# Optimization experiments

Hardware: AMD Instinct MI355X
Metric: run time of the kernel (lower is better)

## Reference

```python
import jax, jax.numpy as jnp
import numpy as np

B, C, W, H, Z = 2, 32, 96, 96, 64
IC = C  # inter_channels defaults to in_channels (required by depthwise g conv)
THRESH = 1.5
EPS = 1e-5


def setup_inputs() -> dict:
    key = jax.random.key(0)
    ks = jax.random.split(key, 12)
    s1 = 1.0 / np.sqrt(C)   # 1x1x1 conv fan-in
    s3 = 1.0 / np.sqrt(3.0) # depthwise (1,1,3) conv fan-in per channel
    return {
        "x": jax.random.normal(ks[0], (B, C, W, H, Z), jnp.float32),
        # per-sample spacings in [0,3): mixes both branches around thresh 1.5
        "spacings": jax.random.uniform(ks[1], (B, 3), jnp.float32) * 3.0,
        "theta_w": jax.random.normal(ks[2], (IC, C), jnp.float32) * s1,
        "theta_b": jax.random.normal(ks[3], (IC,), jnp.float32) * s1,
        "phi_w": jax.random.normal(ks[4], (IC, C), jnp.float32) * s1,
        "phi_b": jax.random.normal(ks[5], (IC,), jnp.float32) * s1,
        "g_w": jax.random.normal(ks[6], (C, 3), jnp.float32) * s3,   # depthwise kernel along z
        "g_b": jax.random.normal(ks[7], (C,), jnp.float32) * s3,
        "W_w": jax.random.normal(ks[8], (C, IC), jnp.float32) * s1,
        "W_b": jax.random.normal(ks[9], (C,), jnp.float32) * s1,
        # torch inits BN gamma=0, beta=0 (zero-init residual trick); use small random
        "bn_gamma": jax.random.normal(ks[10], (C,), jnp.float32) * 0.1,
        "bn_beta": jax.random.normal(ks[11], (C,), jnp.float32) * 0.1,
    }


def _cvec(v):
    return v.reshape(1, -1, 1, 1, 1)


def _conv1x1(h, w, b):
    # 1x1x1 Conv3d == channel-mixing matmul
    return jnp.einsum('bcwhz,oc->bowhz', h, w) + _cvec(b)


def reference(x, spacings, theta_w, theta_b, phi_w, phi_b, g_w, g_b, W_w, W_b, bn_gamma, bn_beta):
    # theta/phi: 1x1x1 convs -> (B, IC, W, H, Z)
    t = _conv1x1(x, theta_w, theta_b)
    p = _conv1x1(x, phi_w, phi_b)

    # g: depthwise conv along z, kernel 3, pad 1 (groups=C)
    xp = jnp.pad(x, ((0, 0), (0, 0), (0, 0), (0, 0), (1, 1)))
    gx = (xp[..., :-2] * _cvec(g_w[:, 0])
          + xp[..., 1:-1] * _cvec(g_w[:, 1])
          + xp[..., 2:] * _cvec(g_w[:, 2])
          + _cvec(g_b))

    # non-local attention along z per (b, w, h) row: scores (B, W, H, Z, Z)
    f = jnp.einsum('bcwhz,bcwhy->bwhzy', t, p)
    a = jax.nn.softmax(f, axis=-1)
    y = jnp.einsum('bwhzy,bcwhy->bcwhz', a, gx)
    nl = y + x  # residual inside compute_x

    # per-sample branch on z-spacing, vectorized with where
    mask = (spacings[:, -1] <= THRESH).reshape(-1, 1, 1, 1, 1)
    res = jnp.where(mask, nl, x)

    # W: 1x1x1 conv + BatchNorm3d (training-mode batch stats)
    out = _conv1x1(res, W_w, W_b)
    mean = jnp.mean(out, axis=(0, 2, 3, 4), keepdims=True)
    var = jnp.var(out, axis=(0, 2, 3, 4), keepdims=True)
    out = (out - mean) * jax.lax.rsqrt(var + EPS)
    return out * _cvec(bn_gamma) + _cvec(bn_beta)
```

## Files before the change

### kernel.cpp

```cpp
#include <hip/hip_runtime.h>
#include <stdint.h>

#define CHS 589824
#define ROWS 18432
#define WHn 9216
#define NRED 1179648.0f
#define LOG2E 1.4426950408889634f

typedef short s16x8 __attribute__((ext_vector_type(8)));
typedef float f32x4v __attribute__((ext_vector_type(4)));

#define MFMA16 __builtin_amdgcn_mfma_f32_16x16x32_bf16

#define WSFRAG 10240

#define OXH 0
#define OP  8704
#define OG  13312
#define LDSZ 17664
#define OO  OP
#define OSC OXH

static __device__ __forceinline__ uint16_t bfh(float v) {
    union { __bf16 h; uint16_t u; } c; c.h = (__bf16)v; return c.u;
}
static __device__ __forceinline__ float bf2f(uint16_t u) {
    union { uint32_t x; float f; } c; c.x = (uint32_t)u << 16; return c.f;
}
static __device__ __forceinline__ uint32_t pk2u(uint16_t a, uint16_t b) {
    return (uint32_t)a | ((uint32_t)b << 16);
}
static __device__ __forceinline__ uint32_t pkbf(float a, float b) {
    return pk2u(bfh(a), bfh(b));
}
static __device__ __forceinline__ float ex2(float x) {
    float r;
    asm("v_exp_f32 %0, %1" : "=v"(r) : "v"(x));
    return r;
}
static __device__ __forceinline__ s16x8 rd8(const char* p) {
    union { uint64_t q[2]; s16x8 s; } v;
    v.q[0] = *(const uint64_t*)p;
    v.q[1] = *(const uint64_t*)(p + 8);
    return v.s;
}

static __device__ __forceinline__ void wfrag2(const float* __restrict__ Wp, int mt, int l15, int kb,
                                              float sc, s16x8& hi, s16x8& lo) {
    const float* p = Wp + (l15 + 16*mt)*32 + 8*kb;
    const float4 f0 = *(const float4*)p;
    const float4 f1 = *(const float4*)(p + 4);
    float f[8] = {f0.x*sc, f0.y*sc, f0.z*sc, f0.w*sc, f1.x*sc, f1.y*sc, f1.z*sc, f1.w*sc};
    union { uint32_t u[4]; s16x8 v; } rh, rl;
    #pragma unroll
    for (int i = 0; i < 4; ++i) {
        const uint16_t h0 = bfh(f[2*i]), h1 = bfh(f[2*i+1]);
        rh.u[i] = pk2u(h0, h1);
        rl.u[i] = pk2u(bfh(f[2*i] - bf2f(h0)), bfh(f[2*i+1] - bf2f(h1)));
    }
    hi = rh.v; lo = rl.v;
}
static __device__ __forceinline__ s16x8 wfragW(const float* __restrict__ Wp, int mt, int l15, int kb) {
    const float* p = Wp + (l15 + 16*mt)*32;
    const float4 f0 = *(const float4*)(p + 4*kb);
    const float4 f1 = *(const float4*)(p + 16 + 4*kb);
    union { uint32_t u[4]; s16x8 v; } r;
    r.u[0] = pkbf(f0.x, f0.y); r.u[1] = pkbf(f0.z, f0.w);
    r.u[2] = pkbf(f1.x, f1.y); r.u[3] = pkbf(f1.z, f1.w);
    return r.v;
}

__global__ __launch_bounds__(256) void k0_frag(
    const float* __restrict__ theta_w, const float* __restrict__ phi_w,
    const float* __restrict__ Ww, char* __restrict__ ws)
{
    const int tid = threadIdx.x;
    const int m = tid >> 7;
    const int r = tid & 127;
    const int mt = r >> 6, l = r & 63;
    s16x8 hi, lo;
    wfrag2(m ? phi_w : theta_w, mt, l & 15, l >> 4, m ? 1.0f : LOG2E, hi, lo);
    *(s16x8*)(ws + m*4096 + (mt*64 + l)*16)        = hi;
    *(s16x8*)(ws + m*4096 + 2048 + (mt*64 + l)*16) = lo;
    if (tid < 128) {
        const int mtw = tid >> 6, lw = tid & 63;
        *(s16x8*)(ws + 8192 + (mtw*64 + lw)*16) = wfragW(Ww, mtw, lw & 15, lw >> 4);
    }
}

__global__ __launch_bounds__(256, 8) void k1_row(
    const float* __restrict__ x, const float* __restrict__ spacings,
    const float* __restrict__ theta_b, const float* __restrict__ phi_b,
    const float* __restrict__ g_w, const float* __restrict__ g_b,
    const float* __restrict__ Wb, const char* __restrict__ frags,
    float* __restrict__ out, float* __restrict__ part)
{
    __shared__ __align__(16) char lds[LDSZ];
    const int t = threadIdx.x;
    const int wv = t >> 6, l = t & 63;
    const int l15 = l & 15, kb = l >> 4;
    const int row = blockIdx.x;
    const int b = row / WHn, wh = row - b*WHn;
    const long base = (long)b*32*CHS + (long)wh*64;
    const int zr = 16*wv + l15;

    float xv[8];
    #pragma unroll
    for (int j = 0; j < 8; ++j) xv[j] = x[base + (long)(8*wv + j)*CHS + l];
    #pragma unroll
    for (int j = 0; j < 4; ++j) {
        const uint16_t h0 = bfh(xv[2*j]), h1 = bfh(xv[2*j+1]);
        *(uint32_t*)(lds + OXH + l*136 + (8*wv + 2*j)*2)      = pk2u(h0, h1);
        *(uint32_t*)(lds + OXH + l*136 + 64 + (8*wv + 2*j)*2) =
            pk2u(bfh(xv[2*j] - bf2f(h0)), bfh(xv[2*j+1] - bf2f(h1)));
    }
    const int pG = 32*(l >> 5) + 8*((l >> 2) & 3) + 4*((l >> 4) & 1) + (l & 3);
    #pragma unroll
    for (int j = 0; j < 8; ++j) {
        const int c = 8*wv + j;
        float xm = __shfl_up(xv[j], 1);   if (l == 0)  xm = 0.f;
        float xp = __shfl_down(xv[j], 1); if (l == 63) xp = 0.f;
        const float g = g_w[3*c]*xm + g_w[3*c+1]*xv[j] + g_w[3*c+2]*xp + g_b[c];
        *(uint16_t*)(lds + OG + c*136 + 2*pG) = bfh(g);
    }
    __syncthreads();

    s16x8 bth, btl;
    {
        const s16x8 bxh = rd8(lds + OXH + zr*136 + 16*kb);
        const s16x8 bxl = rd8(lds + OXH + zr*136 + 64 + 16*kb);
        const s16x8 t0h = *(const s16x8*)(frags + l*16);
        const s16x8 t1h = *(const s16x8*)(frags + 1024 + l*16);
        const s16x8 t0l = *(const s16x8*)(frags + 2048 + l*16);
        const s16x8 t1l = *(const s16x8*)(frags + 3072 + l*16);
        const float4 b0 = *(const float4*)(theta_b + 4*kb);
        const float4 b1 = *(const float4*)(theta_b + 16 + 4*kb);
        f32x4v T0; T0[0]=b0.x*LOG2E; T0[1]=b0.y*LOG2E; T0[2]=b0.z*LOG2E; T0[3]=b0.w*LOG2E;
        f32x4v T1; T1[0]=b1.x*LOG2E; T1[1]=b1.y*LOG2E; T1[2]=b1.z*LOG2E; T1[3]=b1.w*LOG2E;
        T0 = MFMA16(t0h, bxh, T0, 0, 0, 0);
        T0 = MFMA16(t0h, bxl, T0, 0, 0, 0);
        T0 = MFMA16(t0l, bxh, T0, 0, 0, 0);
        T1 = MFMA16(t1h, bxh, T1, 0, 0, 0);
        T1 = MFMA16(t1h, bxl, T1, 0, 0, 0);
        T1 = MFMA16(t1l, bxh, T1, 0, 0, 0);
        const s16x8 p0h = *(const s16x8*)(frags + 4096 + l*16);
        const s16x8 p1h = *(const s16x8*)(frags + 4096 + 1024 + l*16);
        const s16x8 p0l = *(const s16x8*)(frags + 4096 + 2048 + l*16);
        const s16x8 p1l = *(const s16x8*)(frags + 4096 + 3072 + l*16);
        const float4 c0 = *(const float4*)(phi_b + 4*kb);
        const float4 c1 = *(const float4*)(phi_b + 16 + 4*kb);
        f32x4v P0; P0[0]=c0.x; P0[1]=c0.y; P0[2]=c0.z; P0[3]=c0.w;
        f32x4v P1; P1[0]=c1.x; P1[1]=c1.y; P1[2]=c1.z; P1[3]=c1.w;
        P0 = MFMA16(p0h, bxh, P0, 0, 0, 0);
        P0 = MFMA16(p0h, bxl, P0, 0, 0, 0);
        P0 = MFMA16(p0l, bxh, P0, 0, 0, 0);
        P1 = MFMA16(p1h, bxh, P1, 0, 0, 0);
        P1 = MFMA16(p1h, bxl, P1, 0, 0, 0);
        P1 = MFMA16(p1l, bxh, P1, 0, 0, 0);
        union { uint32_t u[2]; uint64_t q; } w;
        w.u[0] = pkbf(P0[0], P0[1]); w.u[1] = pkbf(P0[2], P0[3]);
        *(uint64_t*)(lds + OP + zr*72 + 16*kb) = w.q;
        w.u[0] = pkbf(P1[0], P1[1]); w.u[1] = pkbf(P1[2], P1[3]);
        *(uint64_t*)(lds + OP + zr*72 + 16*kb + 8) = w.q;
        uint16_t h[8];
        #pragma unroll
        for (int r = 0; r < 4; ++r) { h[r] = bfh(T0[r]); h[4+r] = bfh(T1[r]); }
        union { uint32_t u[4]; s16x8 s; } H, L;
        H.u[0] = pk2u(h[0], h[1]); H.u[1] = pk2u(h[2], h[3]);
        H.u[2] = pk2u(h[4], h[5]); H.u[3] = pk2u(h[6], h[7]);
        L.u[0] = pkbf(T0[0]-bf2f(h[0]), T0[1]-bf2f(h[1]));
        L.u[1] = pkbf(T0[2]-bf2f(h[2]), T0[3]-bf2f(h[3]));
        L.u[2] = pkbf(T1[0]-bf2f(h[4]), T1[1]-bf2f(h[5]));
        L.u[3] = pkbf(T1[2]-bf2f(h[6]), T1[3]-bf2f(h[7]));
        bth = H.s; btl = L.s;
    }
    __syncthreads();

    f32x4v Fq[4];
    #pragma unroll
    for (int yt = 0; yt < 4; ++yt) {
        const s16x8 pah = rd8(lds + OP + (16*yt + l15)*72 + 16*kb);
        f32x4v zz; zz[0]=0.f; zz[1]=0.f; zz[2]=0.f; zz[3]=0.f;
        zz = MFMA16(pah, bth, zz, 0, 0, 0);
        zz = MFMA16(pah, btl, zz, 0, 0, 0);
        Fq[yt] = zz;
    }

    s16x8 apk[2];
    float inv;
    {
        float mx = -3.4e38f;
        #pragma unroll
        for (int yt = 0; yt < 4; ++yt)
            #pragma unroll
            for (int r = 0; r < 4; ++r) mx = fmaxf(mx, Fq[yt][r]);
        mx = fmaxf(mx, __shfl_xor(mx, 16));
        mx = fmaxf(mx, __shfl_xor(mx, 32));
        float p[4][4]; float sum = 0.f;
        #pragma unroll
        for (int yt = 0; yt < 4; ++yt)
            #pragma unroll
            for (int r = 0; r < 4; ++r) { p[yt][r] = ex2(Fq[yt][r] - mx); sum += p[yt][r]; }
        sum += __shfl_xor(sum, 16);
        sum += __shfl_xor(sum, 32);
        inv = 1.0f / sum;
        #pragma unroll
        for (int ks = 0; ks < 2; ++ks) {
            union { uint32_t u[4]; s16x8 s; } A;
            A.u[0] = pkbf(p[2*ks][0],   p[2*ks][1]);
            A.u[1] = pkbf(p[2*ks][2],   p[2*ks][3]);
            A.u[2] = pkbf(p[2*ks+1][0], p[2*ks+1][1]);
            A.u[3] = pkbf(p[2*ks+1][2], p[2*ks+1][3]);
            apk[ks] = A.s;
        }
    }

    s16x8 brf;
    {
        f32x4v Yq[2];
        #pragma unroll
        for (int r = 0; r < 4; ++r) { Yq[0][r] = 0.f; Yq[1][r] = 0.f; }
        #pragma unroll
        for (int ks = 0; ks < 2; ++ks) {
            #pragma unroll
            for (int mt = 0; mt < 2; ++mt) {
                const s16x8 gA = rd8(lds + OG + (16*mt + l15)*136 + 64*ks + 16*kb);
                Yq[mt] = MFMA16(gA, apk[ks], Yq[mt], 0, 0, 0);
            }
        }
        const bool msk = spacings[b*3 + 2] <= 1.5f;
        union { uint32_t u[4]; s16x8 s; } R;
        #pragma unroll
        for (int mt = 0; mt < 2; ++mt) {
            const uint64_t xh = *(const uint64_t*)(lds + OXH + zr*136 + (16*mt + 4*kb)*2);
            float rv[4];
            #pragma unroll
            for (int r = 0; r < 4; ++r) {
                const float xr = bf2f((uint16_t)(xh >> (16*r)));
                rv[r] = msk ? fmaf(Yq[mt][r], inv, xr) : xr;
            }
            R.u[2*mt]   = pkbf(rv[0], rv[1]);
            R.u[2*mt+1] = pkbf(rv[2], rv[3]);
        }
        brf = R.s;
    }
    __syncthreads();

    {
        f32x4v accs[2];
        #pragma unroll
        for (int mt = 0; mt < 2; ++mt) {
            const s16x8 aW = *(const s16x8*)(frags + 8192 + (mt*64 + l)*16);
            const float4 wb4 = *(const float4*)(Wb + 16*mt + 4*kb);
            f32x4v acc; acc[0]=wb4.x; acc[1]=wb4.y; acc[2]=wb4.z; acc[3]=wb4.w;
            acc = MFMA16(aW, brf, acc, 0, 0, 0);
            accs[mt] = acc;
            #pragma unroll
            for (int r = 0; r < 4; ++r)
                *(float*)(lds + OO + zr*132 + (16*mt + 4*kb + r)*4) = acc[r];
        }
        float bs[8];
        #pragma unroll
        for (int mt = 0; mt < 2; ++mt)
            #pragma unroll
            for (int r = 0; r < 4; ++r) bs[4*mt+r] = accs[mt][r];
        #pragma unroll
        for (int off = 1; off < 16; off <<= 1)
            #pragma unroll
            for (int i = 0; i < 8; ++i) bs[i] += __shfl_xor(bs[i], off);
        if (l15 == 0) {
            #pragma unroll
            for (int mt = 0; mt < 2; ++mt) {
                union { float f[2]; uint64_t q; } w0, w1;
                w0.f[0] = bs[4*mt]; w0.f[1] = bs[4*mt+1];
                w1.f[0] = bs[4*mt+2]; w1.f[1] = bs[4*mt+3];
                *(uint64_t*)(lds + OSC + wv*256 + (16*mt + 4*kb)*4)     = w0.q;
                *(uint64_t*)(lds + OSC + wv*256 + (16*mt + 4*kb)*4 + 8) = w1.q;
            }
        }
        #pragma unroll
        for (int mt = 0; mt < 2; ++mt)
            #pragma unroll
            for (int r = 0; r < 4; ++r) { const float v = accs[mt][r]; bs[4*mt+r] = v*v; }
        #pragma unroll
        for (int off = 1; off < 16; off <<= 1)
            #pragma unroll
            for (int i = 0; i < 8; ++i) bs[i] += __shfl_xor(bs[i], off);
        if (l15 == 0) {
            #pragma unroll
            for (int mt = 0; mt < 2; ++mt) {
                union { float f[2]; uint64_t q; } w0, w1;
                w0.f[0] = bs[4*mt]; w0.f[1] = bs[4*mt+1];
                w1.f[0] = bs[4*mt+2]; w1.f[1] = bs[4*mt+3];
                *(uint64_t*)(lds + OSC + wv*256 + 128 + (16*mt + 4*kb)*4)     = w0.q;
                *(uint64_t*)(lds + OSC + wv*256 + 128 + (16*mt + 4*kb)*4 + 8) = w1.q;
            }
        }
    }
    __syncthreads();

    #pragma unroll
    for (int k = 0; k < 8; ++k) {
        const int o = wv + 4*k;
        out[base + (long)o*CHS + l] = *(const float*)(lds + OO + l*132 + o*4);
    }
    if (t < 64) {
        const int pl = t >> 5, o = t & 31;
        float s = 0.f;
        #pragma unroll
        for (int w = 0; w < 4; ++w)
            s += *(const float*)(lds + OSC + w*256 + pl*128 + o*4);
        part[row*64 + t] = s;
    }
}

__global__ __launch_bounds__(256) void k2a(const float* __restrict__ part,
                                           float* __restrict__ part2)
{
    __shared__ float red[4][64];
    const int t = threadIdx.x, lane = t & 63, grp = t >> 6;
    const int p = blockIdx.x;
    float s = 0.f;
    for (int k = 0; k < 18; ++k) s += part[(p*72 + grp + 4*k)*64 + lane];
    red[grp][lane] = s;
    __syncthreads();
    if (t < 64) part2[p*64 + t] = red[0][t] + red[1][t] + red[2][t] + red[3][t];
}

__global__ __launch_bounds__(256) void k2b(const float* __restrict__ part2,
    const float* __restrict__ gamma, const float* __restrict__ beta,
    float* __restrict__ sc)
{
    __shared__ float red[4][64];
    __shared__ float tot[64];
    const int t = threadIdx.x, lane = t & 63, grp = t >> 6;
    float s = 0.f;
    for (int k = 0; k < 64; ++k) s += part2[(grp + 4*k)*64 + lane];
    red[grp][lane] = s;
    __syncthreads();
    if (t < 64) tot[t] = red[0][t] + red[1][t] + red[2][t] + red[3][t];
    __syncthreads();
    if (t < 32) {
        const float mean = tot[t] / NRED;
        const float var  = tot[32+t] / NRED - mean*mean;
        const float rstd = rsqrtf(var + 1e-5f);
        const float scale = gamma[t] * rstd;
        sc[t]    = scale;
        sc[32+t] = fmaf(-mean, scale, beta[t]);
    }
}

__global__ __launch_bounds__(256) void k3_norm(float* __restrict__ out,
                                               const float* __restrict__ sc)
{
    __shared__ float s[64];
    if (threadIdx.x < 64) s[threadIdx.x] = sc[threadIdx.x];
    __syncthreads();
    const int total4 = 2*32*CHS/4;
    const int Q = CHS/4;
    for (int i = blockIdx.x*256 + threadIdx.x; i < total4; i += gridDim.x*256) {
        float4 v = ((const float4*)out)[i];
        const int c = (i / Q) & 31;
        const float scale = s[c], shift = s[32+c];
        v.x = fmaf(v.x, scale, shift);
        v.y = fmaf(v.y, scale, shift);
        v.z = fmaf(v.z, scale, shift);
        v.w = fmaf(v.w, scale, shift);
        ((float4*)out)[i] = v;
    }
}

extern "C" void kernel_launch(void* const* d_in, const int* in_sizes, int n_in,
                              void* d_out, int out_size, void* d_ws, size_t ws_size,
                              hipStream_t stream) {
    const float* x        = (const float*)d_in[0];
    const float* spacings = (const float*)d_in[1];
    const float* theta_w  = (const float*)d_in[2];
    const float* theta_b  = (const float*)d_in[3];
    const float* phi_w    = (const float*)d_in[4];
    const float* phi_b    = (const float*)d_in[5];
    const float* g_w      = (const float*)d_in[6];
    const float* g_b      = (const float*)d_in[7];
    const float* Ww       = (const float*)d_in[8];
    const float* Wb       = (const float*)d_in[9];
    const float* gamma    = (const float*)d_in[10];
    const float* beta     = (const float*)d_in[11];
    float* out   = (float*)d_out;
    char*  frags = (char*)d_ws;
    float* part  = (float*)((char*)d_ws + WSFRAG);
    float* part2 = part + ROWS*64;
    float* sc    = part2 + 256*64;

    hipLaunchKernelGGL(k0_frag, dim3(1), dim3(256), 0, stream, theta_w, phi_w, Ww, frags);
    hipLaunchKernelGGL(k1_row, dim3(ROWS), dim3(256), 0, stream,
                       x, spacings, theta_b, phi_b, g_w, g_b, Wb, frags, out, part);
    hipLaunchKernelGGL(k2a, dim3(256), dim3(256), 0, stream, part, part2);
    hipLaunchKernelGGL(k2b, dim3(1), dim3(256), 0, stream, part2, gamma, beta, sc);
    hipLaunchKernelGGL(k3_norm, dim3(4096), dim3(256), 0, stream, out, sc);
}
```

Before: 179.8 us.

## Write W-conv outputs and per-wave partial stats directly to global, drop LDS staging

```diff
diff --git a/kernel.cpp b/kernel.cpp
--- a/kernel.cpp
+++ b/kernel.cpp
@@ -18,8 +18,6 @@
 #define OP  8704
 #define OG  13312
 #define LDSZ 17664
-#define OO  OP
-#define OSC OXH
 
 static __device__ __forceinline__ uint16_t bfh(float v) {
     union { __bf16 h; uint16_t u; } c; c.h = (__bf16)v; return c.u;
@@ -244,7 +242,6 @@
         }
         brf = R.s;
     }
-    __syncthreads();
 
     {
         f32x4v accs[2];
@@ -255,10 +252,14 @@
             f32x4v acc; acc[0]=wb4.x; acc[1]=wb4.y; acc[2]=wb4.z; acc[3]=wb4.w;
             acc = MFMA16(aW, brf, acc, 0, 0, 0);
             accs[mt] = acc;
+        }
+        float* op = out + base + zr;
+        #pragma unroll
+        for (int mt = 0; mt < 2; ++mt)
             #pragma unroll
             for (int r = 0; r < 4; ++r)
-                *(float*)(lds + OO + zr*132 + (16*mt + 4*kb + r)*4) = acc[r];
-        }
+                op[(long)(16*mt + 4*kb + r)*CHS] = accs[mt][r];
+        const int sr = row*4 + wv;
         float bs[8];
         #pragma unroll
         for (int mt = 0; mt < 2; ++mt)
@@ -270,13 +271,10 @@
             for (int i = 0; i < 8; ++i) bs[i] += __shfl_xor(bs[i], off);
         if (l15 == 0) {
             #pragma unroll
-            for (int mt = 0; mt < 2; ++mt) {
-                union { float f[2]; uint64_t q; } w0, w1;
-                w0.f[0] = bs[4*mt]; w0.f[1] = bs[4*mt+1];
-                w1.f[0] = bs[4*mt+2]; w1.f[1] = bs[4*mt+3];
-                *(uint64_t*)(lds + OSC + wv*256 + (16*mt + 4*kb)*4)     = w0.q;
-                *(uint64_t*)(lds + OSC + wv*256 + (16*mt + 4*kb)*4 + 8) = w1.q;
-            }
+            for (int mt = 0; mt < 2; ++mt)
+                #pragma unroll
+                for (int r = 0; r < 4; ++r)
+                    part[sr*64 + 16*mt + 4*kb + r] = bs[4*mt+r];
         }
         #pragma unroll
         for (int mt = 0; mt < 2; ++mt)
@@ -288,29 +286,11 @@
             for (int i = 0; i < 8; ++i) bs[i] += __shfl_xor(bs[i], off);
         if (l15 == 0) {
             #pragma unroll
-            for (int mt = 0; mt < 2; ++mt) {
-                union { float f[2]; uint64_t q; } w0, w1;
-                w0.f[0] = bs[4*mt]; w0.f[1] = bs[4*mt+1];
-                w1.f[0] = bs[4*mt+2]; w1.f[1] = bs[4*mt+3];
-                *(uint64_t*)(lds + OSC + wv*256 + 128 + (16*mt + 4*kb)*4)     = w0.q;
-                *(uint64_t*)(lds + OSC + wv*256 + 128 + (16*mt + 4*kb)*4 + 8) = w1.q;
-            }
-        }
-    }
-    __syncthreads();
-
-    #pragma unroll
-    for (int k = 0; k < 8; ++k) {
-        const int o = wv + 4*k;
-        out[base + (long)o*CHS + l] = *(const float*)(lds + OO + l*132 + o*4);
-    }
-    if (t < 64) {
-        const int pl = t >> 5, o = t & 31;
-        float s = 0.f;
-        #pragma unroll
-        for (int w = 0; w < 4; ++w)
-            s += *(const float*)(lds + OSC + w*256 + pl*128 + o*4);
-        part[row*64 + t] = s;
+            for (int mt = 0; mt < 2; ++mt)
+                #pragma unroll
+                for (int r = 0; r < 4; ++r)
+                    part[sr*64 + 32 + 16*mt + 4*kb + r] = bs[4*mt+r];
+        }
     }
 }
 
@@ -321,7 +301,7 @@
     const int t = threadIdx.x, lane = t & 63, grp = t >> 6;
     const int p = blockIdx.x;
     float s = 0.f;
-    for (int k = 0; k < 18; ++k) s += part[(p*72 + grp + 4*k)*64 + lane];
+    for (int k = 0; k < 72; ++k) s += part[(p*288 + grp + 4*k)*64 + lane];
     red[grp][lane] = s;
     __syncthreads();
     if (t < 64) part2[p*64 + t] = red[0][t] + red[1][t] + red[2][t] + red[3][t];
@@ -388,7 +368,7 @@
     float* out   = (float*)d_out;
     char*  frags = (char*)d_ws;
     float* part  = (float*)((char*)d_ws + WSFRAG);
-    float* part2 = part + ROWS*64;
+    float* part2 = part + (size_t)ROWS*256;
     float* sc    = part2 + 256*64;
 
     hipLaunchKernelGGL(k0_frag, dim3(1), dim3(256), 0, stream, theta_w, phi_w, Ww, frags);
```

Result: slower. 184.6 us (+2.7%).
